# Optimization experiments

Measured on AMD Instinct MI355X. Metric: run time of the kernel, lower is better.

Reference implementation:

```python
import jax, jax.numpy as jnp
import numpy as np

N_NODES = 20000
DIM = 512
N_EDGES = 320000
EPS = 1e-12  # torch F.normalize eps


def setup_inputs() -> dict:
    key = jax.random.key(0)
    k = jax.random.split(key, 6)
    scale = 1.0 / np.sqrt(DIM)
    return {
        "x": jax.random.normal(k[0], (N_NODES, DIM), dtype=jnp.float32),
        "edge_index": jax.random.randint(k[1], (2, N_EDGES), 0, N_NODES, dtype=jnp.int64),
        "W1": jax.random.normal(k[2], (DIM, DIM), dtype=jnp.float32) * scale,
        "b1": jnp.zeros((DIM,), dtype=jnp.float32),
        "W2": jax.random.normal(k[3], (DIM, DIM), dtype=jnp.float32) * scale,
        "b2": jnp.zeros((DIM,), dtype=jnp.float32),
        "alpha": jax.random.uniform(k[4], (), dtype=jnp.float32),
    }


def _gcn_conv(x, src, dst, norm, W, b, n):
    # x: [N, D]; src/dst: [E+N] (with self-loops); norm: [E+N]
    h = x @ W                              # [N, D] linear (no bias, like PyG lin)
    msg = h[src] * norm[:, None]           # gather + edgewise scale  [E+N, D]
    agg = jax.ops.segment_sum(msg, dst, num_segments=n)  # scatter-add [N, D]
    return agg + b


def _prep_edges(edge_index, n):
    loops = jnp.arange(n, dtype=edge_index.dtype)
    src = jnp.concatenate([edge_index[0], loops])
    dst = jnp.concatenate([edge_index[1], loops])
    deg = jax.ops.segment_sum(jnp.ones_like(dst, dtype=jnp.float32), dst, num_segments=n)
    dinv = jnp.where(deg > 0, jax.lax.rsqrt(deg), 0.0)
    norm = dinv[src] * dinv[dst]           # symmetric deg^{-1/2} normalization
    return src, dst, norm


def reference(x, edge_index, W1, b1, W2, b2, alpha):
    n = x.shape[0]
    src, dst, norm = _prep_edges(edge_index, n)
    h = _gcn_conv(x, src, dst, norm, W1, b1, n)
    h = jax.nn.relu(h)
    # dropout: eval mode -> identity
    h = _gcn_conv(h, src, dst, norm, W2, b2, n)
    a = jnp.clip(alpha, -1.0, 1.0)
    y = x + a * h
    nrm = jnp.maximum(jnp.linalg.norm(y, axis=-1, keepdims=True), EPS)
    return y / nrm
```

## Files before the change

kernel.cpp:

```cpp
#include <hip/hip_runtime.h>
#include <stdint.h>

#define DIMC 512
#define CAP 64

typedef __bf16 bf16_t;
typedef bf16_t bf16x8 __attribute__((ext_vector_type(8)));
typedef float f32x4 __attribute__((ext_vector_type(4)));
typedef float f32x2 __attribute__((ext_vector_type(2)));

__device__ __forceinline__ float4 ld4(const float* p) { return *(const float4*)p; }

typedef __attribute__((address_space(1))) void gvoid;
typedef __attribute__((address_space(3))) void svoid;

__device__ __forceinline__ void gload_lds16(const void* g, void* l) {
    __builtin_amdgcn_global_load_lds((gvoid*)(uintptr_t)g,
                                     (svoid*)(uint32_t)(uintptr_t)l, 16, 0, 0);
}

__device__ __forceinline__ uint8_t enc_fp8(float v) {
    return (uint8_t)(__builtin_amdgcn_cvt_pk_fp8_f32(v, v, 0, false) & 0xff);
}
__device__ __forceinline__ void dec8_fma(float* acc, uint2 u, float w) {
    f32x2 p0 = __builtin_amdgcn_cvt_pk_f32_fp8((int)u.x, false);
    f32x2 p1 = __builtin_amdgcn_cvt_pk_f32_fp8((int)u.x, true);
    f32x2 p2 = __builtin_amdgcn_cvt_pk_f32_fp8((int)u.y, false);
    f32x2 p3 = __builtin_amdgcn_cvt_pk_f32_fp8((int)u.y, true);
    acc[0] += p0.x * w; acc[1] += p0.y * w;
    acc[2] += p1.x * w; acc[3] += p1.y * w;
    acc[4] += p2.x * w; acc[5] += p2.y * w;
    acc[6] += p3.x * w; acc[7] += p3.y * w;
}

__global__ __launch_bounds__(256) void zero_kernel(int4* __restrict__ p, int n4) {
    int i = blockIdx.x * 256 + threadIdx.x;
    if (i < n4) p[i] = make_int4(0, 0, 0, 0);
}

__global__ __launch_bounds__(256) void prep_kernel(const float* __restrict__ x,
        bf16_t* __restrict__ xb, const float* __restrict__ W1,
        const float* __restrict__ W2, bf16_t* __restrict__ W1t,
        bf16_t* __restrict__ W2t, int n8, int nb_f2b,
        const int* __restrict__ ei, int E,
        int* __restrict__ cursor, int* __restrict__ csr) {
    __shared__ float tile[32][33];
    int b = blockIdx.x;
    if (b < nb_f2b) {
        int base = b * 2048 + threadIdx.x;
        #pragma unroll
        for (int it = 0; it < 8; ++it) {
            int i = base + it * 256;
            if (i < n8) {
                const float4* p = (const float4*)x + (size_t)i * 2;
                float4 a = p[0], c = p[1];
                bf16x8 o;
                o[0] = (bf16_t)a.x; o[1] = (bf16_t)a.y; o[2] = (bf16_t)a.z; o[3] = (bf16_t)a.w;
                o[4] = (bf16_t)c.x; o[5] = (bf16_t)c.y; o[6] = (bf16_t)c.z; o[7] = (bf16_t)c.w;
                ((bf16x8*)xb)[i] = o;
            }
        }
        return;
    }
    if (b < nb_f2b + 256) {
        int sub = b - nb_f2b;
        int bx = sub & 15, by = sub >> 4;
        int tx = threadIdx.x & 31, ty = threadIdx.x >> 5;
        #pragma unroll
        for (int which = 0; which < 2; ++which) {
            const float* W = which ? W2 : W1;
            bf16_t* Wt = which ? W2t : W1t;
            if (which) __syncthreads();
            for (int j = ty; j < 32; j += 8)
                tile[j][tx] = W[(size_t)(by * 32 + j) * DIMC + bx * 32 + tx];
            __syncthreads();
            for (int j = ty; j < 32; j += 8)
                Wt[(size_t)(bx * 32 + j) * DIMC + by * 32 + tx] = (bf16_t)tile[tx][j];
        }
        return;
    }
    int base = (b - nb_f2b - 256) * 1024 + threadIdx.x;
    #pragma unroll
    for (int it = 0; it < 4; ++it) {
        int e = base + it * 256;
        if (e < E) {
            int s = ei[e], d = ei[E + e];
            int pos = atomicAdd(&cursor[d], 1);
            if (pos < CAP) csr[(size_t)d * CAP + pos] = s;
        }
    }
}

template<bool FP8OUT>
__global__ __launch_bounds__(256) void gemm_mfma(const bf16_t* __restrict__ A,
        const bf16_t* __restrict__ Bt, void* __restrict__ Cout, int M) {
    __shared__ bf16_t As[2 * 8192];
    __shared__ bf16_t Bs[2 * 8192];
    const int t = threadIdx.x;
    const int lane = t & 63, wid = t >> 6;

    int nwg = gridDim.x * gridDim.y;
    int lin = blockIdx.y * gridDim.x + blockIdx.x;
    int q = nwg >> 3, r = nwg & 7;
    int k = lin & 7, i = lin >> 3;
    int mk = (k < r) ? k : r;
    int orig = k * q + mk + i;
    int bx2 = orig & 3, by2 = orig >> 2;
    const int m0 = by2 * 128, n0 = bx2 * 128;

    const bf16_t* asrc[4];
    const bf16_t* bsrc[4];
    int ldoff[4];
    #pragma unroll
    for (int q2 = 0; q2 < 4; ++q2) {
        int off = q2 * 4096 + wid * 1024 + lane * 16;
        int rr = off >> 7;
        int p = (off >> 4) & 7;
        int c = p ^ (rr & 7);
        int ga = m0 + rr; if (ga > M - 1) ga = M - 1;
        asrc[q2] = A + (size_t)ga * DIMC + c * 8;
        bsrc[q2] = Bt + (size_t)(n0 + rr) * DIMC + c * 8;
        ldoff[q2] = q2 * 4096 + wid * 1024;
    }

    const int wr = wid >> 1, wc = wid & 1;
    int aoff[4][2], boff[4][2];
    #pragma unroll
    for (int i2 = 0; i2 < 4; ++i2) {
        int ra = wr * 64 + i2 * 16 + (lane & 15);
        int rb = wc * 64 + i2 * 16 + (lane & 15);
        #pragma unroll
        for (int ks = 0; ks < 2; ++ks) {
            int ca = ks * 4 + (lane >> 4);
            aoff[i2][ks] = ra * 128 + (ca ^ (ra & 7)) * 16;
            boff[i2][ks] = rb * 128 + (ca ^ (rb & 7)) * 16;
        }
    }

    #pragma unroll
    for (int q2 = 0; q2 < 4; ++q2) {
        gload_lds16(asrc[q2], (char*)As + ldoff[q2]);
        gload_lds16(bsrc[q2], (char*)Bs + ldoff[q2]);
    }

    f32x4 acc[4][4] = {};
    int cur = 0;
    for (int k0 = 0; k0 < DIMC; k0 += 64) {
        __syncthreads();
        if (k0 + 64 < DIMC) {
            int nxt = cur ^ 1;
            #pragma unroll
            for (int q2 = 0; q2 < 4; ++q2) {
                gload_lds16(asrc[q2] + k0 + 64, (char*)As + nxt * 16384 + ldoff[q2]);
                gload_lds16(bsrc[q2] + k0 + 64, (char*)Bs + nxt * 16384 + ldoff[q2]);
            }
        }
        const char* Ab = (const char*)As + cur * 16384;
        const char* Bb = (const char*)Bs + cur * 16384;
        #pragma unroll
        for (int ks = 0; ks < 2; ++ks) {
            bf16x8 av[4], bv[4];
            #pragma unroll
            for (int i2 = 0; i2 < 4; ++i2) av[i2] = *(const bf16x8*)(Ab + aoff[i2][ks]);
            #pragma unroll
            for (int j = 0; j < 4; ++j) bv[j] = *(const bf16x8*)(Bb + boff[j][ks]);
            #pragma unroll
            for (int i2 = 0; i2 < 4; ++i2)
                #pragma unroll
                for (int j = 0; j < 4; ++j)
                    acc[i2][j] = __builtin_amdgcn_mfma_f32_16x16x32_bf16(av[i2], bv[j], acc[i2][j], 0, 0, 0);
        }
        cur ^= 1;
    }

    #pragma unroll
    for (int i2 = 0; i2 < 4; ++i2) {
        int rbase = m0 + wr * 64 + i2 * 16 + (lane >> 4) * 4;
        #pragma unroll
        for (int rr = 0; rr < 4; ++rr) {
            int row = rbase + rr;
            if (row < M) {
                #pragma unroll
                for (int j = 0; j < 4; ++j) {
                    int col = n0 + wc * 64 + j * 16 + (lane & 15);
                    if (FP8OUT)
                        ((uint8_t*)Cout)[(size_t)row * DIMC + col] = enc_fp8(acc[i2][j][rr]);
                    else
                        ((bf16_t*)Cout)[(size_t)row * DIMC + col] = (bf16_t)acc[i2][j][rr];
                }
            }
        }
    }
}

__global__ __launch_bounds__(256) void agg_relu_kernel(const uint8_t* __restrict__ H8,
        const int* __restrict__ csr, const int* __restrict__ cursor,
        const float* __restrict__ bias, bf16_t* __restrict__ G, int n) {
    int node = (blockIdx.x * blockDim.x + threadIdx.x) >> 6;
    if (node >= n) return;
    int lane = threadIdx.x & 63;
    int c0 = lane * 8;
    int deg = cursor[node];
    float dv = rsqrtf((float)(deg + 1));
    int dl = (deg < CAP) ? deg : CAP;
    const uint8_t* Hc = H8 + c0;
    float acc[8] = {};
    dec8_fma(acc, *(const uint2*)(Hc + (size_t)node * DIMC), dv);
    const int* crow = csr + (size_t)node * CAP;
    int e = 0;
    for (; e + 8 <= dl; e += 8) {
        int idx[8]; float wt[8]; uint2 r[8];
        #pragma unroll
        for (int j = 0; j < 8; ++j) idx[j] = crow[e + j];
        #pragma unroll
        for (int j = 0; j < 8; ++j) wt[j] = rsqrtf((float)(cursor[idx[j]] + 1));
        #pragma unroll
        for (int j = 0; j < 8; ++j) r[j] = *(const uint2*)(Hc + (size_t)idx[j] * DIMC);
        #pragma unroll
        for (int j = 0; j < 8; ++j) dec8_fma(acc, r[j], wt[j]);
    }
    for (; e < dl; ++e) {
        int s0 = crow[e];
        float w0 = rsqrtf((float)(cursor[s0] + 1));
        dec8_fma(acc, *(const uint2*)(Hc + (size_t)s0 * DIMC), w0);
    }
    float4 b0 = ld4(bias + c0), b1 = ld4(bias + c0 + 4);
    float bb[8] = {b0.x, b0.y, b0.z, b0.w, b1.x, b1.y, b1.z, b1.w};
    bf16x8 o;
    #pragma unroll
    for (int j = 0; j < 8; ++j) o[j] = (bf16_t)fmaxf(dv * acc[j] + bb[j], 0.f);
    *(bf16x8*)(G + (size_t)node * DIMC + c0) = o;
}

__global__ __launch_bounds__(256) void agg_final_kernel(const uint8_t* __restrict__ H8,
        const bf16_t* __restrict__ xb, const int* __restrict__ csr,
        const int* __restrict__ cursor, const float* __restrict__ bias,
        const float* __restrict__ alphaPtr, float* __restrict__ out, int n) {
    int node = (blockIdx.x * blockDim.x + threadIdx.x) >> 6;
    if (node >= n) return;
    int lane = threadIdx.x & 63;
    int c0 = lane * 8;
    int deg = cursor[node];
    float dv = rsqrtf((float)(deg + 1));
    int dl = (deg < CAP) ? deg : CAP;
    const uint8_t* Hc = H8 + c0;
    float acc[8] = {};
    dec8_fma(acc, *(const uint2*)(Hc + (size_t)node * DIMC), dv);
    const int* crow = csr + (size_t)node * CAP;
    int e = 0;
    for (; e + 8 <= dl; e += 8) {
        int idx[8]; float wt[8]; uint2 r[8];
        #pragma unroll
        for (int j = 0; j < 8; ++j) idx[j] = crow[e + j];
        #pragma unroll
        for (int j = 0; j < 8; ++j) wt[j] = rsqrtf((float)(cursor[idx[j]] + 1));
        #pragma unroll
        for (int j = 0; j < 8; ++j) r[j] = *(const uint2*)(Hc + (size_t)idx[j] * DIMC);
        #pragma unroll
        for (int j = 0; j < 8; ++j) dec8_fma(acc, r[j], wt[j]);
    }
    for (; e < dl; ++e) {
        int s0 = crow[e];
        float w0 = rsqrtf((float)(cursor[s0] + 1));
        dec8_fma(acc, *(const uint2*)(Hc + (size_t)s0 * DIMC), w0);
    }
    float al = alphaPtr[0];
    al = fminf(fmaxf(al, -1.f), 1.f);
    float4 b0 = ld4(bias + c0), b1 = ld4(bias + c0 + 4);
    float bb[8] = {b0.x, b0.y, b0.z, b0.w, b1.x, b1.y, b1.z, b1.w};
    bf16x8 xv = *(const bf16x8*)(xb + (size_t)node * DIMC + c0);
    float y[8];
    float ss = 0.f;
    #pragma unroll
    for (int j = 0; j < 8; ++j) {
        y[j] = (float)xv[j] + al * (dv * acc[j] + bb[j]);
        ss += y[j] * y[j];
    }
    #pragma unroll
    for (int off = 1; off < 64; off <<= 1) ss += __shfl_xor(ss, off);
    float sc = 1.f / fmaxf(sqrtf(ss), 1e-12f);
    float* op = out + (size_t)node * DIMC + c0;
    *(float4*)op = make_float4(y[0] * sc, y[1] * sc, y[2] * sc, y[3] * sc);
    *(float4*)(op + 4) = make_float4(y[4] * sc, y[5] * sc, y[6] * sc, y[7] * sc);
}

extern "C" void kernel_launch(void* const* d_in, const int* in_sizes, int n_in,
                              void* d_out, int out_size, void* d_ws, size_t ws_size,
                              hipStream_t stream) {
    const float* x     = (const float*)d_in[0];
    const int*   ei    = (const int*)d_in[1];
    const float* W1    = (const float*)d_in[2];
    const float* b1    = (const float*)d_in[3];
    const float* W2    = (const float*)d_in[4];
    const float* b2    = (const float*)d_in[5];
    const float* alpha = (const float*)d_in[6];
    float* out = (float*)d_out;

    const int N = in_sizes[0] / DIMC;
    const int E = in_sizes[1] / 2;
    const size_t MN = (size_t)N * DIMC;

    char* w = (char*)d_ws;
    auto carve = [&](size_t bytes) {
        void* p = (void*)w;
        w += (bytes + 255) & ~(size_t)255;
        return p;
    };
    uint8_t* H8a   = (uint8_t*)carve(MN);
    uint8_t* H8b   = (uint8_t*)carve(MN);
    bf16_t* Gb     = (bf16_t*)carve(MN * sizeof(bf16_t));
    bf16_t* xb     = (bf16_t*)carve(MN * sizeof(bf16_t));
    bf16_t* W1t    = (bf16_t*)carve((size_t)DIMC * DIMC * sizeof(bf16_t));
    bf16_t* W2t    = (bf16_t*)carve((size_t)DIMC * DIMC * sizeof(bf16_t));
    int*    cursor = (int*)carve(((size_t)N + 4) * sizeof(int));
    int*    csr    = (int*)carve((size_t)N * CAP * sizeof(int));

    int n4 = (N + 3) / 4;
    zero_kernel<<<(n4 + 255) / 256, 256, 0, stream>>>((int4*)cursor, n4);

    int n8 = (int)(MN / 8);
    int nb_f2b = (n8 + 2047) / 2048;
    int nb_fill = (E + 1023) / 1024;
    prep_kernel<<<nb_f2b + 256 + nb_fill, 256, 0, stream>>>(
        x, xb, W1, W2, W1t, W2t, n8, nb_f2b, ei, E, cursor, csr);

    dim3 gg(DIMC / 128, (N + 127) / 128);
    int aggBlocks = (N + 3) / 4;
    gemm_mfma<true><<<gg, 256, 0, stream>>>(xb, W1t, (void*)H8a, N);
    agg_relu_kernel<<<aggBlocks, 256, 0, stream>>>(H8a, csr, cursor, b1, Gb, N);
    gemm_mfma<true><<<gg, 256, 0, stream>>>(Gb, W2t, (void*)H8b, N);
    agg_final_kernel<<<aggBlocks, 256, 0, stream>>>(H8b, xb, csr, cursor, b2, alpha, out, N);
}
```

Before: 125.0 us.

## Precompute per-edge source normalization weights into packed CSR records

Splits CSR construction into a degree-count pass and a second fill pass that stores (src, rsqrt(deg_src+1)) pairs per edge. The aggregation kernels then read the weight directly instead of doing a dependent gather of the source degree, which removes one level of pointer chasing per edge. A 4-wide batch is added before the scalar tail. In exchange there is an extra kernel launch and edge pass, and the CSR is twice as large to read.

After: 140.5 us. 1.12x slower.

```diff
diff --git a/kernel.cpp b/kernel.cpp
--- a/kernel.cpp
+++ b/kernel.cpp
@@ -42,8 +42,7 @@
         bf16_t* __restrict__ xb, const float* __restrict__ W1,
         const float* __restrict__ W2, bf16_t* __restrict__ W1t,
         bf16_t* __restrict__ W2t, int n8, int nb_f2b,
-        const int* __restrict__ ei, int E,
-        int* __restrict__ cursor, int* __restrict__ csr) {
+        const int* __restrict__ ei, int E, int* __restrict__ cnt) {
     __shared__ float tile[32][33];
     int b = blockIdx.x;
     if (b < nb_f2b) {
@@ -83,10 +82,22 @@
     #pragma unroll
     for (int it = 0; it < 4; ++it) {
         int e = base + it * 256;
+        if (e < E) atomicAdd(&cnt[ei[E + e]], 1);
+    }
+}
+
+__global__ __launch_bounds__(256) void fill2_kernel(const int* __restrict__ ei, int E,
+        const int* __restrict__ cnt, int* __restrict__ cursor2,
+        int2* __restrict__ csr2) {
+    int base = blockIdx.x * 1024 + threadIdx.x;
+    #pragma unroll
+    for (int it = 0; it < 4; ++it) {
+        int e = base + it * 256;
         if (e < E) {
             int s = ei[e], d = ei[E + e];
-            int pos = atomicAdd(&cursor[d], 1);
-            if (pos < CAP) csr[(size_t)d * CAP + pos] = s;
+            float w = rsqrtf((float)(cnt[s] + 1));
+            int pos = atomicAdd(&cursor2[d], 1);
+            if (pos < CAP) csr2[(size_t)d * CAP + pos] = make_int2(s, __float_as_int(w));
         }
     }
 }
@@ -193,36 +204,37 @@
     }
 }
 
+#define GATHER_BATCH(NB)                                                            \
+    for (; e + NB <= dl; e += NB) {                                                 \
+        int2 rec[NB]; uint2 rv[NB];                                                 \
+        _Pragma("unroll")                                                           \
+        for (int j = 0; j < NB; ++j) rec[j] = crow[e + j];                          \
+        _Pragma("unroll")                                                           \
+        for (int j = 0; j < NB; ++j) rv[j] = *(const uint2*)(Hc + (size_t)rec[j].x * DIMC); \
+        _Pragma("unroll")                                                           \
+        for (int j = 0; j < NB; ++j) dec8_fma(acc, rv[j], __int_as_float(rec[j].y)); \
+    }
+
 __global__ __launch_bounds__(256) void agg_relu_kernel(const uint8_t* __restrict__ H8,
-        const int* __restrict__ csr, const int* __restrict__ cursor,
+        const int2* __restrict__ csr2, const int* __restrict__ cnt,
         const float* __restrict__ bias, bf16_t* __restrict__ G, int n) {
     int node = (blockIdx.x * blockDim.x + threadIdx.x) >> 6;
     if (node >= n) return;
     int lane = threadIdx.x & 63;
     int c0 = lane * 8;
-    int deg = cursor[node];
+    int deg = cnt[node];
     float dv = rsqrtf((float)(deg + 1));
     int dl = (deg < CAP) ? deg : CAP;
     const uint8_t* Hc = H8 + c0;
     float acc[8] = {};
     dec8_fma(acc, *(const uint2*)(Hc + (size_t)node * DIMC), dv);
-    const int* crow = csr + (size_t)node * CAP;
+    const int2* crow = csr2 + (size_t)node * CAP;
     int e = 0;
-    for (; e + 8 <= dl; e += 8) {
-        int idx[8]; float wt[8]; uint2 r[8];
-        #pragma unroll
-        for (int j = 0; j < 8; ++j) idx[j] = crow[e + j];
-        #pragma unroll
-        for (int j = 0; j < 8; ++j) wt[j] = rsqrtf((float)(cursor[idx[j]] + 1));
-        #pragma unroll
-        for (int j = 0; j < 8; ++j) r[j] = *(const uint2*)(Hc + (size_t)idx[j] * DIMC);
-        #pragma unroll
-        for (int j = 0; j < 8; ++j) dec8_fma(acc, r[j], wt[j]);
-    }
+    GATHER_BATCH(8)
+    GATHER_BATCH(4)
     for (; e < dl; ++e) {
-        int s0 = crow[e];
-        float w0 = rsqrtf((float)(cursor[s0] + 1));
-        dec8_fma(acc, *(const uint2*)(Hc + (size_t)s0 * DIMC), w0);
+        int2 rec = crow[e];
+        dec8_fma(acc, *(const uint2*)(Hc + (size_t)rec.x * DIMC), __int_as_float(rec.y));
     }
     float4 b0 = ld4(bias + c0), b1 = ld4(bias + c0 + 4);
     float bb[8] = {b0.x, b0.y, b0.z, b0.w, b1.x, b1.y, b1.z, b1.w};
@@ -233,36 +245,26 @@
 }
 
 __global__ __launch_bounds__(256) void agg_final_kernel(const uint8_t* __restrict__ H8,
-        const bf16_t* __restrict__ xb, const int* __restrict__ csr,
-        const int* __restrict__ cursor, const float* __restrict__ bias,
+        const bf16_t* __restrict__ xb, const int2* __restrict__ csr2,
+        const int* __restrict__ cnt, const float* __restrict__ bias,
         const float* __restrict__ alphaPtr, float* __restrict__ out, int n) {
     int node = (blockIdx.x * blockDim.x + threadIdx.x) >> 6;
     if (node >= n) return;
     int lane = threadIdx.x & 63;
     int c0 = lane * 8;
-    int deg = cursor[node];
+    int deg = cnt[node];
     float dv = rsqrtf((float)(deg + 1));
     int dl = (deg < CAP) ? deg : CAP;
     const uint8_t* Hc = H8 + c0;
     float acc[8] = {};
     dec8_fma(acc, *(const uint2*)(Hc + (size_t)node * DIMC), dv);
-    const int* crow = csr + (size_t)node * CAP;
+    const int2* crow = csr2 + (size_t)node * CAP;
     int e = 0;
-    for (; e + 8 <= dl; e += 8) {
-        int idx[8]; float wt[8]; uint2 r[8];
-        #pragma unroll
-        for (int j = 0; j < 8; ++j) idx[j] = crow[e + j];
-        #pragma unroll
-        for (int j = 0; j < 8; ++j) wt[j] = rsqrtf((float)(cursor[idx[j]] + 1));
-        #pragma unroll
-        for (int j = 0; j < 8; ++j) r[j] = *(const uint2*)(Hc + (size_t)idx[j] * DIMC);
-        #pragma unroll
-        for (int j = 0; j < 8; ++j) dec8_fma(acc, r[j], wt[j]);
-    }
+    GATHER_BATCH(8)
+    GATHER_BATCH(4)
     for (; e < dl; ++e) {
-        int s0 = crow[e];
-        float w0 = rsqrtf((float)(cursor[s0] + 1));
-        dec8_fma(acc, *(const uint2*)(Hc + (size_t)s0 * DIMC), w0);
+        int2 rec = crow[e];
+        dec8_fma(acc, *(const uint2*)(Hc + (size_t)rec.x * DIMC), __int_as_float(rec.y));
     }
     float al = alphaPtr[0];
     al = fminf(fmaxf(al, -1.f), 1.f);
@@ -299,6 +301,7 @@
     const int N = in_sizes[0] / DIMC;
     const int E = in_sizes[1] / 2;
     const size_t MN = (size_t)N * DIMC;
+    const int Npad = (N + 63) & ~63;
 
     char* w = (char*)d_ws;
     auto carve = [&](size_t bytes) {
@@ -306,28 +309,31 @@
         w += (bytes + 255) & ~(size_t)255;
         return p;
     };
-    uint8_t* H8a   = (uint8_t*)carve(MN);
-    uint8_t* H8b   = (uint8_t*)carve(MN);
-    bf16_t* Gb     = (bf16_t*)carve(MN * sizeof(bf16_t));
-    bf16_t* xb     = (bf16_t*)carve(MN * sizeof(bf16_t));
-    bf16_t* W1t    = (bf16_t*)carve((size_t)DIMC * DIMC * sizeof(bf16_t));
-    bf16_t* W2t    = (bf16_t*)carve((size_t)DIMC * DIMC * sizeof(bf16_t));
-    int*    cursor = (int*)carve(((size_t)N + 4) * sizeof(int));
-    int*    csr    = (int*)carve((size_t)N * CAP * sizeof(int));
-
-    int n4 = (N + 3) / 4;
-    zero_kernel<<<(n4 + 255) / 256, 256, 0, stream>>>((int4*)cursor, n4);
+    uint8_t* H8a    = (uint8_t*)carve(MN);
+    uint8_t* H8b    = (uint8_t*)carve(MN);
+    bf16_t* Gb      = (bf16_t*)carve(MN * sizeof(bf16_t));
+    bf16_t* xb      = (bf16_t*)carve(MN * sizeof(bf16_t));
+    bf16_t* W1t     = (bf16_t*)carve((size_t)DIMC * DIMC * sizeof(bf16_t));
+    bf16_t* W2t     = (bf16_t*)carve((size_t)DIMC * DIMC * sizeof(bf16_t));
+    int*    cnt     = (int*)carve((size_t)2 * Npad * sizeof(int));
+    int*    cursor2 = cnt + Npad;
+    int2*   csr2    = (int2*)carve((size_t)N * CAP * sizeof(int2));
+
+    int n4 = (2 * Npad) / 4;
+    zero_kernel<<<(n4 + 255) / 256, 256, 0, stream>>>((int4*)cnt, n4);
 
     int n8 = (int)(MN / 8);
     int nb_f2b = (n8 + 2047) / 2048;
     int nb_fill = (E + 1023) / 1024;
     prep_kernel<<<nb_f2b + 256 + nb_fill, 256, 0, stream>>>(
-        x, xb, W1, W2, W1t, W2t, n8, nb_f2b, ei, E, cursor, csr);
+        x, xb, W1, W2, W1t, W2t, n8, nb_f2b, ei, E, cnt);
+
+    fill2_kernel<<<nb_fill, 256, 0, stream>>>(ei, E, cnt, cursor2, csr2);
 
     dim3 gg(DIMC / 128, (N + 127) / 128);
     int aggBlocks = (N + 3) / 4;
     gemm_mfma<true><<<gg, 256, 0, stream>>>(xb, W1t, (void*)H8a, N);
-    agg_relu_kernel<<<aggBlocks, 256, 0, stream>>>(H8a, csr, cursor, b1, Gb, N);
+    agg_relu_kernel<<<aggBlocks, 256, 0, stream>>>(H8a, csr2, cnt, b1, Gb, N);
     gemm_mfma<true><<<gg, 256, 0, stream>>>(Gb, W2t, (void*)H8b, N);
-    agg_final_kernel<<<aggBlocks, 256, 0, stream>>>(H8b, xb, csr, cursor, b2, alpha, out, N);
-}
+    agg_final_kernel<<<aggBlocks, 256, 0, stream>>>(H8b, xb, csr2, cnt, b2, alpha, out, N);
+}
```
